# Performance work log

Hardware: AMD Instinct MI355X
Metric: run time of the kernel (lower is better)

The kernel has to match this reference:

```python
import jax, jax.numpy as jnp
import numpy as np

DIM = 64
HEADS = 4
DIM_HEAD = 32
HIDDEN = HEADS * DIM_HEAD  # 128
EPS = 1e-5


def _layernorm_ch(x, g, b):
    # channel-dim LayerNorm (biased var), x: [b, c, n]
    mean = jnp.mean(x, axis=1, keepdims=True)
    var = jnp.var(x, axis=1, keepdims=True)  # unbiased=False
    return (x - mean) / jnp.sqrt(var + EPS) * g.reshape(1, -1, 1) + b.reshape(1, -1, 1)


def setup_inputs() -> dict:
    key = jax.random.key(0)
    ks = jax.random.split(key, 4)
    x = jax.random.normal(ks[0], (2, DIM, 32, 64, 64), dtype=jnp.float32)
    # 1x1x1 convs are channel matmuls; store weights as [out_ch, in_ch]
    w_qkv = jax.random.normal(ks[1], (HIDDEN * 3, DIM), dtype=jnp.float32) * (1.0 / np.sqrt(DIM))
    w_out = jax.random.normal(ks[2], (DIM, HIDDEN), dtype=jnp.float32) * (1.0 / np.sqrt(HIDDEN))
    b_out = jax.random.normal(ks[3], (DIM,), dtype=jnp.float32) * 0.02
    g1 = jnp.ones((DIM,), dtype=jnp.float32)
    b1 = jnp.zeros((DIM,), dtype=jnp.float32)
    g2 = jnp.ones((DIM,), dtype=jnp.float32)
    b2 = jnp.zeros((DIM,), dtype=jnp.float32)
    return {"x": x, "g1": g1, "b1": b1, "w_qkv": w_qkv, "w_out": w_out,
            "b_out": b_out, "g2": g2, "b2": b2}


def reference(x, g1, b1, w_qkv, w_out, b_out, g2, b2):
    b, c, *spatial = x.shape
    n = int(np.prod(spatial))
    scale = DIM_HEAD ** -0.5

    xf = x.reshape(b, c, n)
    xn = _layernorm_ch(xf, g1, b1)

    # 1x1x1 conv qkv projection (no bias)
    qkv = jnp.einsum('oc,bcn->bon', w_qkv, xn)  # [b, 3*hidden, n]
    qkv = qkv.reshape(b, 3, HEADS, DIM_HEAD, n)
    q, k, v = qkv[:, 0], qkv[:, 1], qkv[:, 2]   # each [b, h, d, n]

    q = jax.nn.softmax(q, axis=2) * scale       # softmax over dim_head
    k = jax.nn.softmax(k, axis=3)               # softmax over tokens

    ctx = jnp.einsum('bhdn,bhen->bhde', k, v)   # [b, h, d, e] small
    out = jnp.einsum('bhde,bhdn->bhen', ctx, q) # [b, h, e, n]
    out = out.reshape(b, HIDDEN, n)

    y = jnp.einsum('oc,bcn->bon', w_out, out) + b_out.reshape(1, -1, 1)
    y = _layernorm_ch(y, g2, b2)
    return y.reshape(b, c, *spatial)
```

## Files before the change

kernel.cpp:

```cpp
#include <hip/hip_runtime.h>

#define NCOL 131072
#define CH 64

typedef float floatx4 __attribute__((ext_vector_type(4)));
typedef __bf16 bf16x8 __attribute__((ext_vector_type(8)));
typedef unsigned int u32x4 __attribute__((ext_vector_type(4)));
typedef unsigned int u32x2 __attribute__((ext_vector_type(2)));

union FragU { u32x4 q; bf16x8 v; unsigned short us[8]; };

__device__ __forceinline__ unsigned short bfb(float f){
  union { __bf16 h; unsigned short s; } u; u.h = (__bf16)f; return u.s;
}
__device__ __forceinline__ float bf2f(unsigned short h){
  union { unsigned u; float f; } x{(unsigned)h << 16};
  return x.f;
}

__device__ __forceinline__ void ln_stage(const float* __restrict__ xp,
    const float* __restrict__ g, const float* __restrict__ bb,
    unsigned short* __restrict__ xn_s, int t, unsigned short* __restrict__ xg)
{
  float xv[64]; float s = 0.f, ss = 0.f;
  #pragma unroll
  for (int c = 0; c < 64; c++){ float u = xp[(long)c*NCOL]; xv[c] = u; s += u; ss = fmaf(u,u,ss); }
  const float mean = s * (1.f/64.f);
  const float rstd = rsqrtf(ss * (1.f/64.f) - mean*mean + 1e-5f);
  #pragma unroll
  for (int c = 0; c < 64; c++) xv[c] = (xv[c]-mean)*rstd*g[c] + bb[c];
  #pragma unroll
  for (int j = 0; j < 8; j++){
    FragU u;
    #pragma unroll
    for (int e = 0; e < 8; e++) u.v[e] = (__bf16)xv[j*8+e];
    *(u32x4*)(xn_s + t*72 + j*8) = u.q;
    if (xg) *(u32x4*)(xg + j*8) = u.q;
  }
}

__global__ __launch_bounds__(256) void kW(
    const float* __restrict__ wqkv, unsigned short* __restrict__ wbf, float* __restrict__ Oz)
{
  const int i = blockIdx.x*256 + threadIdx.x;
  wbf[i] = bfb(wqkv[i]);
  if (i < 8448) Oz[i] = 0.f;
}

__global__ __launch_bounds__(256) void kA(
    const float* __restrict__ x, const float* __restrict__ g1, const float* __restrict__ b1,
    const unsigned short* __restrict__ wbf, float* __restrict__ pctx, float* __restrict__ Zg,
    unsigned short* __restrict__ xng)
{
  __shared__ __align__(16) char smem[37888];
  unsigned short* xn_s = (unsigned short*)smem;
  unsigned short* ek_s = (unsigned short*)smem;
  unsigned short* v_s  = (unsigned short*)(smem + 16896);
  float* Zp            = (float*)(smem + 33792);

  const int t = threadIdx.x;
  const int bid = blockIdx.x;
  const int b = bid >> 9;
  const long col0 = (long)(bid & 511) * 256;
  const int w = t >> 6, lane = t & 63, qq = lane >> 4, l16 = lane & 15;

  ln_stage(x + (long)b*CH*NCOL + col0 + t, g1, b1, xn_s, t,
           xng ? xng + ((long)b*NCOL + col0 + t)*64 : (unsigned short*)nullptr);
  FragU bx[4][2];
  #pragma unroll
  for (int nt = 0; nt < 4; nt++)
    #pragma unroll
    for (int ks = 0; ks < 2; ks++)
      bx[nt][ks].q = *(const u32x4*)(xn_s + ((4*w+nt)*16 + l16)*72 + ks*32 + qq*8);
  __syncthreads();

  floatx4 cc[4][2][2];
  #pragma unroll
  for (int h = 0; h < 4; h++)
    #pragma unroll
    for (int dt = 0; dt < 2; dt++)
      #pragma unroll
      for (int et = 0; et < 2; et++)
        cc[h][dt][et] = floatx4{0.f,0.f,0.f,0.f};

  #pragma unroll
  for (int h = 0; h < 4; h++){
    float zr[8];
    #pragma unroll
    for (int j = 0; j < 8; j++) zr[j] = 0.f;
    #pragma unroll
    for (int rt = 0; rt < 4; rt++){
      const int row0 = ((rt < 2) ? 128 : 256) + h*32 + (rt & 1)*16;
      const unsigned short* wr = wbf + (row0 + l16)*64 + qq*8;
      FragU a0, a1;
      a0.q = *(const u32x4*)wr;
      a1.q = *(const u32x4*)(wr + 32);
      unsigned short* dst = ((rt < 2) ? ek_s : v_s) + ((rt & 1)*16 + qq*4)*264;
      #pragma unroll
      for (int nt = 0; nt < 4; nt++){
        floatx4 c = floatx4{0.f,0.f,0.f,0.f};
        c = __builtin_amdgcn_mfma_f32_16x16x32_bf16(a0.v, bx[nt][0].v, c, 0, 0, 0);
        c = __builtin_amdgcn_mfma_f32_16x16x32_bf16(a1.v, bx[nt][1].v, c, 0, 0, 0);
        const int colb = (4*w+nt)*16 + l16;
        if (rt < 2){
          #pragma unroll
          for (int r = 0; r < 4; r++){
            const float e = __expf(c[r]);
            dst[r*264 + colb] = bfb(e);
            zr[(rt & 1)*4 + r] += e;
          }
        } else {
          #pragma unroll
          for (int r = 0; r < 4; r++) dst[r*264 + colb] = bfb(c[r]);
        }
      }
    }
    #pragma unroll
    for (int j = 0; j < 8; j++){
      float v = zr[j];
      v += __shfl_xor(v, 1, 64); v += __shfl_xor(v, 2, 64);
      v += __shfl_xor(v, 4, 64); v += __shfl_xor(v, 8, 64);
      if (l16 == 0) Zp[w*128 + h*32 + (j >> 2)*16 + qq*4 + (j & 3)] = v;
    }
    #pragma unroll
    for (int kk = 0; kk < 2; kk++){
      const int ks2 = 2*w + kk;
      FragU ae[2], bv[2];
      #pragma unroll
      for (int dt = 0; dt < 2; dt++) ae[dt].q = *(const u32x4*)(ek_s + (dt*16 + l16)*264 + ks2*32 + qq*8);
      #pragma unroll
      for (int et = 0; et < 2; et++) bv[et].q = *(const u32x4*)(v_s + (et*16 + l16)*264 + ks2*32 + qq*8);
      #pragma unroll
      for (int dt = 0; dt < 2; dt++)
        #pragma unroll
        for (int et = 0; et < 2; et++)
          cc[h][dt][et] = __builtin_amdgcn_mfma_f32_16x16x32_bf16(ae[dt].v, bv[et].v, cc[h][dt][et], 0, 0, 0);
    }
  }
  __syncthreads();

  if (t < 128){
    const float z = Zp[t] + Zp[128 + t] + Zp[256 + t] + Zp[384 + t];
    atomicAdd(&Zg[b*128 + t], z);
  }

  float* scr = (float*)smem;
  if (w & 1){
    #pragma unroll
    for (int h = 0; h < 4; h++)
      #pragma unroll
      for (int dt = 0; dt < 2; dt++)
        #pragma unroll
        for (int et = 0; et < 2; et++)
          ((floatx4*)scr)[(w>>1)*1024 + (h*4 + dt*2 + et)*64 + lane] = cc[h][dt][et];
  }
  __syncthreads();
  if (!(w & 1)){
    #pragma unroll
    for (int h = 0; h < 4; h++)
      #pragma unroll
      for (int dt = 0; dt < 2; dt++)
        #pragma unroll
        for (int et = 0; et < 2; et++)
          cc[h][dt][et] += ((floatx4*)scr)[(w>>1)*1024 + (h*4 + dt*2 + et)*64 + lane];
  }
  __syncthreads();
  if (w == 2){
    #pragma unroll
    for (int h = 0; h < 4; h++)
      #pragma unroll
      for (int dt = 0; dt < 2; dt++)
        #pragma unroll
        for (int et = 0; et < 2; et++)
          ((floatx4*)scr)[(h*4 + dt*2 + et)*64 + lane] = cc[h][dt][et];
  }
  __syncthreads();
  if (w == 0){
    #pragma unroll
    for (int h = 0; h < 4; h++)
      #pragma unroll
      for (int dt = 0; dt < 2; dt++)
        #pragma unroll
        for (int et = 0; et < 2; et++){
          floatx4 r = cc[h][dt][et] + ((floatx4*)scr)[(h*4 + dt*2 + et)*64 + lane];
          *(floatx4*)(pctx + (long)bid*4096 + (h*4 + dt*2 + et)*256 + lane*4) = r;
        }
  }
}

__global__ __launch_bounds__(256) void kR1(
    const float* __restrict__ pctx, float* __restrict__ O)
{
  const int blk = blockIdx.x;
  const int b = blk >> 7;
  const int part = (blk >> 4) & 7;
  const int chunk = blk & 15;
  const int t = threadIdx.x;
  const int r = chunk*256 + t;
  const float* p = pctx + ((long)(b*512 + part*64))*4096 + r;
  float s = 0.f;
  #pragma unroll 16
  for (int row = 0; row < 64; row++) s += p[(long)row*4096];
  atomicAdd(&O[b*4096 + r], s);
}

__device__ __forceinline__ void kB_body(
    const unsigned short* __restrict__ wbf, const float* __restrict__ O,
    const float* __restrict__ Zg, const float* __restrict__ wout,
    float* __restrict__ y, char* smem, const FragU bx[4][2],
    int t, int b, long col0, int w, int lane, int qq, int l16)
{
  float* O_s           = (float*)smem;
  unsigned short* qs_s = (unsigned short*)smem;
  unsigned short* Mg_s = (unsigned short*)(smem + 20480);
  float* sp            = (float*)(smem + 36864);

  {
    const float* Ob = O + (long)b*4096;
    #pragma unroll
    for (int j = 0; j < 4; j++)
      ((floatx4*)O_s)[j*256 + t] = ((const floatx4*)Ob)[j*256 + t];
    __syncthreads();

    const int h = t >> 6, o = t & 63;
    float wrow[32];
    #pragma unroll
    for (int ee = 0; ee < 32; ee++) wrow[ee] = wout[o*128 + h*32 + ee];
    #pragma unroll
    for (int j2 = 0; j2 < 16; j2++){
      float m01[2];
      #pragma unroll
      for (int half = 0; half < 2; half++){
        const int dd = j2*2 + half;
        const int dt = dd >> 4, qq2 = (dd >> 2) & 3, rg2 = dd & 3;
        float m = 0.f;
        #pragma unroll
        for (int ee = 0; ee < 32; ee++){
          const int et = ee >> 4, l16e = ee & 15;
          m = fmaf(wrow[ee], O_s[h*1024 + (dt*2+et)*256 + (qq2*16+l16e)*4 + rg2], m);
        }
        m01[half] = m / Zg[b*128 + h*32 + dd];
      }
      *(unsigned*)(Mg_s + (h*64 + o)*32 + j2*2) =
          (unsigned)bfb(m01[0]) | ((unsigned)bfb(m01[1]) << 16);
    }
  }
  __syncthreads();

  floatx4 yacc[4][4];
  #pragma unroll
  for (int ot = 0; ot < 4; ot++)
    #pragma unroll
    for (int nt = 0; nt < 4; nt++)
      yacc[ot][nt] = floatx4{0.f,0.f,0.f,0.f};

  #pragma unroll
  for (int h = 0; h < 4; h++){
    FragU a00, a01, a10, a11;
    {
      const unsigned short* wr0 = wbf + (h*32 + l16)*64 + qq*8;
      const unsigned short* wr1 = wbf + (h*32 + 16 + l16)*64 + qq*8;
      a00.q = *(const u32x4*)wr0; a01.q = *(const u32x4*)(wr0 + 32);
      a10.q = *(const u32x4*)wr1; a11.q = *(const u32x4*)(wr1 + 32);
    }
    #pragma unroll
    for (int nt = 0; nt < 4; nt++){
      floatx4 c0 = floatx4{0.f,0.f,0.f,0.f};
      floatx4 c1 = floatx4{0.f,0.f,0.f,0.f};
      c0 = __builtin_amdgcn_mfma_f32_16x16x32_bf16(a00.v, bx[nt][0].v, c0, 0, 0, 0);
      c0 = __builtin_amdgcn_mfma_f32_16x16x32_bf16(a01.v, bx[nt][1].v, c0, 0, 0, 0);
      c1 = __builtin_amdgcn_mfma_f32_16x16x32_bf16(a10.v, bx[nt][0].v, c1, 0, 0, 0);
      c1 = __builtin_amdgcn_mfma_f32_16x16x32_bf16(a11.v, bx[nt][1].v, c1, 0, 0, 0);
      float e[8]; float s = 0.f;
      #pragma unroll
      for (int r = 0; r < 4; r++){ e[r] = __expf(c0[r]); s += e[r]; }
      #pragma unroll
      for (int r = 0; r < 4; r++){ e[4+r] = __expf(c1[r]); s += e[4+r]; }
      s += __shfl_xor(s, 16, 64); s += __shfl_xor(s, 32, 64);
      const float sc = 0.17677669529663687f / s;
      const int colb = (4*w+nt)*16 + l16;
      u32x2 pk0, pk1;
      pk0[0] = (unsigned)bfb(e[0]*sc) | ((unsigned)bfb(e[1]*sc) << 16);
      pk0[1] = (unsigned)bfb(e[2]*sc) | ((unsigned)bfb(e[3]*sc) << 16);
      pk1[0] = (unsigned)bfb(e[4]*sc) | ((unsigned)bfb(e[5]*sc) << 16);
      pk1[1] = (unsigned)bfb(e[6]*sc) | ((unsigned)bfb(e[7]*sc) << 16);
      *(u32x2*)(qs_s + colb*40 + qq*4)      = pk0;
      *(u32x2*)(qs_s + colb*40 + 16 + qq*4) = pk1;
    }
    #pragma unroll
    for (int ot = 0; ot < 4; ot++){
      FragU am;
      am.q = *(const u32x4*)(Mg_s + (h*64 + ot*16 + l16)*32 + qq*8);
      #pragma unroll
      for (int nt = 0; nt < 4; nt++){
        FragU bq; bq.q = *(const u32x4*)(qs_s + ((4*w+nt)*16 + l16)*40 + qq*8);
        yacc[ot][nt] = __builtin_amdgcn_mfma_f32_16x16x32_bf16(am.v, bq.v, yacc[ot][nt], 0, 0, 0);
      }
    }
  }

  const long ybase = (long)b*CH*NCOL;
  #pragma unroll
  for (int nt = 0; nt < 4; nt++){
    const long colg = col0 + (4*w+nt)*16 + l16;
    float vals[16]; float s = 0.f, ss = 0.f;
    #pragma unroll
    for (int ot = 0; ot < 4; ot++)
      #pragma unroll
      for (int r = 0; r < 4; r++){
        const float v = yacc[ot][nt][r] + sp[ot*16 + qq*4 + r];
        vals[ot*4+r] = v; s += v; ss = fmaf(v, v, ss);
      }
    s  += __shfl_xor(s, 16, 64);  s  += __shfl_xor(s, 32, 64);
    ss += __shfl_xor(ss, 16, 64); ss += __shfl_xor(ss, 32, 64);
    const float mean = s * (1.f/64.f);
    const float rstd = rsqrtf(ss * (1.f/64.f) - mean*mean + 1e-5f);
    #pragma unroll
    for (int ot = 0; ot < 4; ot++)
      #pragma unroll
      for (int r = 0; r < 4; r++){
        const int row = ot*16 + qq*4 + r;
        y[ybase + (long)row*NCOL + colg] = (vals[ot*4+r]-mean)*rstd*sp[64+row] + sp[128+row];
      }
  }
}

__global__ __launch_bounds__(256) void kBf(
    const float* __restrict__ x, const float* __restrict__ g1, const float* __restrict__ b1,
    const unsigned short* __restrict__ wbf, const float* __restrict__ O,
    const float* __restrict__ Zg, const float* __restrict__ wout,
    const float* __restrict__ bout, const float* __restrict__ g2, const float* __restrict__ b2,
    float* __restrict__ y)
{
  __shared__ __align__(16) char smem[37632];
  unsigned short* xn_s = (unsigned short*)smem;
  float* sp            = (float*)(smem + 36864);

  const int t = threadIdx.x;
  const int bid = blockIdx.x;
  const int b = bid >> 9;
  const long col0 = (long)(bid & 511) * 256;
  const int w = t >> 6, lane = t & 63, qq = lane >> 4, l16 = lane & 15;

  if (t < 64){ sp[t] = bout[t]; sp[64+t] = g2[t]; sp[128+t] = b2[t]; }
  ln_stage(x + (long)b*CH*NCOL + col0 + t, g1, b1, xn_s, t, (unsigned short*)nullptr);
  FragU bx[4][2];
  #pragma unroll
  for (int nt = 0; nt < 4; nt++)
    #pragma unroll
    for (int ks = 0; ks < 2; ks++)
      bx[nt][ks].q = *(const u32x4*)(xn_s + ((4*w+nt)*16 + l16)*72 + ks*32 + qq*8);
  __syncthreads();

  kB_body(wbf, O, Zg, wout, y, smem, bx, t, b, col0, w, lane, qq, l16);
}

__global__ __launch_bounds__(256) void kBs(
    const unsigned short* __restrict__ xng,
    const unsigned short* __restrict__ wbf, const float* __restrict__ O,
    const float* __restrict__ Zg, const float* __restrict__ wout,
    const float* __restrict__ bout, const float* __restrict__ g2, const float* __restrict__ b2,
    float* __restrict__ y)
{
  __shared__ __align__(16) char smem[37632];
  float* sp = (float*)(smem + 36864);

  const int t = threadIdx.x;
  const int bid = blockIdx.x;
  const int b = bid >> 9;
  const long col0 = (long)(bid & 511) * 256;
  const int w = t >> 6, lane = t & 63, qq = lane >> 4, l16 = lane & 15;

  if (t < 64){ sp[t] = bout[t]; sp[64+t] = g2[t]; sp[128+t] = b2[t]; }
  FragU bx[4][2];
  #pragma unroll
  for (int nt = 0; nt < 4; nt++){
    const unsigned short* xr = xng + ((long)b*NCOL + col0 + (4*w+nt)*16 + l16)*64;
    #pragma unroll
    for (int ks = 0; ks < 2; ks++)
      bx[nt][ks].q = *(const u32x4*)(xr + ks*32 + qq*8);
  }

  kB_body(wbf, O, Zg, wout, y, smem, bx, t, b, col0, w, lane, qq, l16);
}

extern "C" void kernel_launch(void* const* d_in, const int* in_sizes, int n_in,
                              void* d_out, int out_size, void* d_ws, size_t ws_size,
                              hipStream_t stream)
{
  const float* x    = (const float*)d_in[0];
  const float* g1   = (const float*)d_in[1];
  const float* b1   = (const float*)d_in[2];
  const float* wqkv = (const float*)d_in[3];
  const float* wout = (const float*)d_in[4];
  const float* bout = (const float*)d_in[5];
  const float* g2   = (const float*)d_in[6];
  const float* b2   = (const float*)d_in[7];
  float* y  = (float*)d_out;
  float* ws = (float*)d_ws;

  float* pctx = ws;
  float* O    = ws + 4194304;
  float* Zg   = ws + 4202496;
  unsigned short* wbf = (unsigned short*)(ws + 4202752);
  unsigned short* xng = (unsigned short*)(ws + 4215040);
  const bool big = ws_size >= (size_t)12603648 * 4;

  hipLaunchKernelGGL(kW,  dim3(96),   dim3(256), 0, stream, wqkv, wbf, O);
  hipLaunchKernelGGL(kA,  dim3(1024), dim3(256), 0, stream, x, g1, b1, wbf, pctx, Zg,
                     big ? xng : (unsigned short*)nullptr);
  hipLaunchKernelGGL(kR1, dim3(256),  dim3(256), 0, stream, pctx, O);
  if (big)
    hipLaunchKernelGGL(kBs, dim3(1024), dim3(256), 0, stream, xng, wbf, O, Zg, wout, bout, g2, b2, y);
  else
    hipLaunchKernelGGL(kBf, dim3(1024), dim3(256), 0, stream, x, g1, b1, wbf, O, Zg, wout, bout, g2, b2, y);
}
```

Baseline: 237.6 us.

## Hoist per-batch output-projection matrix into separate small kernel

Before, every one of the 1024 blocks in the final kernel rebuilt the per-batch fused matrix (w_out times context, divided by Z) from O, redoing about 1M FMAs per block. A new tiny kernel kM computes this bf16 matrix once per batch into workspace that reuses the pctx region. The final kernels now just load 16KB from global into LDS. The cost is one extra launch and a round trip of the matrix through global memory.

```diff
diff --git a/kernel.cpp b/kernel.cpp
--- a/kernel.cpp
+++ b/kernel.cpp
@@ -204,47 +204,37 @@
   atomicAdd(&O[b*4096 + r], s);
 }
 
-__device__ __forceinline__ void kB_body(
-    const unsigned short* __restrict__ wbf, const float* __restrict__ O,
-    const float* __restrict__ Zg, const float* __restrict__ wout,
+__global__ __launch_bounds__(256) void kM(
+    const float* __restrict__ O, const float* __restrict__ Zg,
+    const float* __restrict__ wout, unsigned short* __restrict__ Mgbf)
+{
+  const int idx = blockIdx.x*256 + threadIdx.x;
+  const int b = idx >> 13, rem = idx & 8191;
+  const int h = rem >> 11, o = (rem >> 5) & 63, dd = rem & 31;
+  const int dt = dd >> 4, qq = (dd >> 2) & 3, rg = dd & 3;
+  float m = 0.f;
+  #pragma unroll
+  for (int ee = 0; ee < 32; ee++){
+    const int et = ee >> 4, l16 = ee & 15;
+    const int r = h*1024 + (dt*2 + et)*256 + (qq*16 + l16)*4 + rg;
+    m = fmaf(wout[o*128 + h*32 + ee], O[b*4096 + r], m);
+  }
+  m /= Zg[b*128 + h*32 + dd];
+  Mgbf[idx] = bfb(m);
+}
+
+__device__ __forceinline__ void kC_body(
+    const unsigned short* __restrict__ wbf, const unsigned short* __restrict__ Mgbf,
     float* __restrict__ y, char* smem, const FragU bx[4][2],
     int t, int b, long col0, int w, int lane, int qq, int l16)
 {
-  float* O_s           = (float*)smem;
   unsigned short* qs_s = (unsigned short*)smem;
   unsigned short* Mg_s = (unsigned short*)(smem + 20480);
   float* sp            = (float*)(smem + 36864);
 
-  {
-    const float* Ob = O + (long)b*4096;
-    #pragma unroll
-    for (int j = 0; j < 4; j++)
-      ((floatx4*)O_s)[j*256 + t] = ((const floatx4*)Ob)[j*256 + t];
-    __syncthreads();
-
-    const int h = t >> 6, o = t & 63;
-    float wrow[32];
-    #pragma unroll
-    for (int ee = 0; ee < 32; ee++) wrow[ee] = wout[o*128 + h*32 + ee];
-    #pragma unroll
-    for (int j2 = 0; j2 < 16; j2++){
-      float m01[2];
-      #pragma unroll
-      for (int half = 0; half < 2; half++){
-        const int dd = j2*2 + half;
-        const int dt = dd >> 4, qq2 = (dd >> 2) & 3, rg2 = dd & 3;
-        float m = 0.f;
-        #pragma unroll
-        for (int ee = 0; ee < 32; ee++){
-          const int et = ee >> 4, l16e = ee & 15;
-          m = fmaf(wrow[ee], O_s[h*1024 + (dt*2+et)*256 + (qq2*16+l16e)*4 + rg2], m);
-        }
-        m01[half] = m / Zg[b*128 + h*32 + dd];
-      }
-      *(unsigned*)(Mg_s + (h*64 + o)*32 + j2*2) =
-          (unsigned)bfb(m01[0]) | ((unsigned)bfb(m01[1]) << 16);
-    }
-  }
+  #pragma unroll
+  for (int j = 0; j < 4; j++)
+    ((u32x4*)Mg_s)[j*256 + t] = ((const u32x4*)(Mgbf + (long)b*8192))[j*256 + t];
   __syncthreads();
 
   floatx4 yacc[4][4];
@@ -325,16 +315,14 @@
   }
 }
 
-__global__ __launch_bounds__(256) void kBf(
-    const float* __restrict__ x, const float* __restrict__ g1, const float* __restrict__ b1,
-    const unsigned short* __restrict__ wbf, const float* __restrict__ O,
-    const float* __restrict__ Zg, const float* __restrict__ wout,
+__global__ __launch_bounds__(256) void kCs(
+    const unsigned short* __restrict__ xng, const unsigned short* __restrict__ wbf,
+    const unsigned short* __restrict__ Mgbf,
     const float* __restrict__ bout, const float* __restrict__ g2, const float* __restrict__ b2,
     float* __restrict__ y)
 {
   __shared__ __align__(16) char smem[37632];
-  unsigned short* xn_s = (unsigned short*)smem;
-  float* sp            = (float*)(smem + 36864);
+  float* sp = (float*)(smem + 36864);
 
   const int t = threadIdx.x;
   const int bid = blockIdx.x;
@@ -343,27 +331,26 @@
   const int w = t >> 6, lane = t & 63, qq = lane >> 4, l16 = lane & 15;
 
   if (t < 64){ sp[t] = bout[t]; sp[64+t] = g2[t]; sp[128+t] = b2[t]; }
-  ln_stage(x + (long)b*CH*NCOL + col0 + t, g1, b1, xn_s, t, (unsigned short*)nullptr);
   FragU bx[4][2];
   #pragma unroll
-  for (int nt = 0; nt < 4; nt++)
+  for (int nt = 0; nt < 4; nt++){
+    const unsigned short* xr = xng + ((long)b*NCOL + col0 + (4*w+nt)*16 + l16)*64;
     #pragma unroll
     for (int ks = 0; ks < 2; ks++)
-      bx[nt][ks].q = *(const u32x4*)(xn_s + ((4*w+nt)*16 + l16)*72 + ks*32 + qq*8);
-  __syncthreads();
-
-  kB_body(wbf, O, Zg, wout, y, smem, bx, t, b, col0, w, lane, qq, l16);
-}
-
-__global__ __launch_bounds__(256) void kBs(
-    const unsigned short* __restrict__ xng,
-    const unsigned short* __restrict__ wbf, const float* __restrict__ O,
-    const float* __restrict__ Zg, const float* __restrict__ wout,
+      bx[nt][ks].q = *(const u32x4*)(xr + ks*32 + qq*8);
+  }
+  kC_body(wbf, Mgbf, y, smem, bx, t, b, col0, w, lane, qq, l16);
+}
+
+__global__ __launch_bounds__(256) void kCf(
+    const float* __restrict__ x, const float* __restrict__ g1, const float* __restrict__ b1,
+    const unsigned short* __restrict__ wbf, const unsigned short* __restrict__ Mgbf,
     const float* __restrict__ bout, const float* __restrict__ g2, const float* __restrict__ b2,
     float* __restrict__ y)
 {
   __shared__ __align__(16) char smem[37632];
-  float* sp = (float*)(smem + 36864);
+  unsigned short* xn_s = (unsigned short*)smem;
+  float* sp            = (float*)(smem + 36864);
 
   const int t = threadIdx.x;
   const int bid = blockIdx.x;
@@ -372,16 +359,15 @@
   const int w = t >> 6, lane = t & 63, qq = lane >> 4, l16 = lane & 15;
 
   if (t < 64){ sp[t] = bout[t]; sp[64+t] = g2[t]; sp[128+t] = b2[t]; }
+  ln_stage(x + (long)b*CH*NCOL + col0 + t, g1, b1, xn_s, t, (unsigned short*)nullptr);
   FragU bx[4][2];
   #pragma unroll
-  for (int nt = 0; nt < 4; nt++){
-    const unsigned short* xr = xng + ((long)b*NCOL + col0 + (4*w+nt)*16 + l16)*64;
+  for (int nt = 0; nt < 4; nt++)
     #pragma unroll
     for (int ks = 0; ks < 2; ks++)
-      bx[nt][ks].q = *(const u32x4*)(xr + ks*32 + qq*8);
-  }
-
-  kB_body(wbf, O, Zg, wout, y, smem, bx, t, b, col0, w, lane, qq, l16);
+      bx[nt][ks].q = *(const u32x4*)(xn_s + ((4*w+nt)*16 + l16)*72 + ks*32 + qq*8);
+  __syncthreads();
+  kC_body(wbf, Mgbf, y, smem, bx, t, b, col0, w, lane, qq, l16);
 }
 
 extern "C" void kernel_launch(void* const* d_in, const int* in_sizes, int n_in,
@@ -400,6 +386,7 @@
   float* ws = (float*)d_ws;
 
   float* pctx = ws;
+  unsigned short* Mgbf = (unsigned short*)ws;
   float* O    = ws + 4194304;
   float* Zg   = ws + 4202496;
   unsigned short* wbf = (unsigned short*)(ws + 4202752);
@@ -410,8 +397,9 @@
   hipLaunchKernelGGL(kA,  dim3(1024), dim3(256), 0, stream, x, g1, b1, wbf, pctx, Zg,
                      big ? xng : (unsigned short*)nullptr);
   hipLaunchKernelGGL(kR1, dim3(256),  dim3(256), 0, stream, pctx, O);
+  hipLaunchKernelGGL(kM,  dim3(64),   dim3(256), 0, stream, O, Zg, wout, Mgbf);
   if (big)
-    hipLaunchKernelGGL(kBs, dim3(1024), dim3(256), 0, stream, xng, wbf, O, Zg, wout, bout, g2, b2, y);
+    hipLaunchKernelGGL(kCs, dim3(1024), dim3(256), 0, stream, xng, wbf, Mgbf, bout, g2, b2, y);
   else
-    hipLaunchKernelGGL(kBf, dim3(1024), dim3(256), 0, stream, x, g1, b1, wbf, O, Zg, wout, bout, g2, b2, y);
-}
+    hipLaunchKernelGGL(kCf, dim3(1024), dim3(256), 0, stream, x, g1, b1, wbf, Mgbf, bout, g2, b2, y);
+}
```

Result: faster. 203.0 us (-14.6%).
